# Performance work log

Hardware: AMD Instinct MI355X
Metric: run time of the kernel (lower is better)

Reference implementation:

```python
import jax, jax.numpy as jnp
import numpy as np

# MLP widths: 2 -> 1024 -> 512 -> 256 -> 3, ReLU between layers (not after last)
DIMS = [2, 1024, 512, 256, 3]


def setup_inputs() -> dict:
    key = jax.random.key(0)
    ks = jax.random.split(key, 1 + 2 * (len(DIMS) - 1))
    N = 262144  # 512x512 pixel coordinates
    inp = {"coord": jax.random.normal(ks[0], (N, 2), dtype=jnp.float32)}
    # PyTorch nn.Linear default init: U(-1/sqrt(fan_in), 1/sqrt(fan_in))
    for i, (fi, fo) in enumerate(zip(DIMS[:-1], DIMS[1:])):
        bound = 1.0 / np.sqrt(fi)
        inp[f"W{i}"] = jax.random.uniform(ks[1 + 2 * i], (fi, fo), jnp.float32, -bound, bound)
        inp[f"b{i}"] = jax.random.uniform(ks[2 + 2 * i], (fo,), jnp.float32, -bound, bound)
    return inp


def reference(coord, W0, b0, W1, b1, W2, b2, W3, b3):
    h = jax.nn.relu(coord @ W0 + b0)   # [N, 1024]
    h = jax.nn.relu(h @ W1 + b1)       # [N, 512]
    h = jax.nn.relu(h @ W2 + b2)       # [N, 256]
    return h @ W3 + b3                 # [N, 3]
```

## Files before the change

kernel.cpp:

```cpp
#include <hip/hip_runtime.h>


typedef _Float16 f16;
typedef f16 f16x8 __attribute__((ext_vector_type(8)));
typedef f16 f16x4 __attribute__((ext_vector_type(4)));
typedef float f32x16 __attribute__((ext_vector_type(16)));

#define MFMA(a, b, c) __builtin_amdgcn_mfma_f32_32x32x16_f16((a), (b), (c), 0, 0, 0)

#define U_W1F 0
#define U_W2F 65536
#define U_W3F 81920
#define U_P0F 82944
#define U_B1F 84992
#define U_B2F 86016
#define U_TOTAL 86528

__global__ void prep_kernel(const float* __restrict__ W0, const float* __restrict__ b0,
                            const float* __restrict__ W1, const float* __restrict__ b1,
                            const float* __restrict__ W2, const float* __restrict__ b2,
                            const float* __restrict__ W3, f16* __restrict__ ws)
{
    int u = blockIdx.x * 256 + threadIdx.x;
    if (u >= U_TOTAL) return;
    int lane = u & 63;
    int l31 = lane & 31;
    int q = lane >> 5;
    f16x8 v;
#pragma unroll
    for (int e = 0; e < 8; ++e) v[e] = (f16)0.f;

    if (u < U_W2F) {
        int jt = u >> 12, ks = (u >> 6) & 63;
        int j = jt * 32 + l31;
        int kb = ks * 16 + q * 8;
        const float* p = W1 + (size_t)kb * 512 + j;
#pragma unroll
        for (int e = 0; e < 8; ++e) v[e] = (f16)p[(size_t)e * 512];
    } else if (u < U_W3F) {
        int t = u - U_W2F;
        int jt = t >> 11, ks = (t >> 6) & 31;
        int j = jt * 32 + l31;
        int kb = ks * 16 + q * 8;
        const float* p = W2 + (size_t)kb * 256 + j;
#pragma unroll
        for (int e = 0; e < 8; ++e) v[e] = (f16)p[(size_t)e * 256];
    } else if (u < U_P0F) {
        int t = u - U_W3F;
        int ks = t >> 6;
        int j = l31;
        int kb = ks * 16 + q * 8;
        if (j < 3) {
            const float* p = W3 + (size_t)kb * 3 + j;
#pragma unroll
            for (int e = 0; e < 8; ++e) v[e] = (f16)p[(size_t)e * 3];
        }
    } else if (u < U_B1F) {
        int t = u - U_P0F;
        int jt = t >> 6;
        int j = jt * 32 + l31;
        if (q == 0) {
            float w00 = W0[j], w01 = W0[1024 + j], bb = b0[j];
            f16 w00h = (f16)w00, w01h = (f16)w01, bh = (f16)bb;
            v[0] = w00h; v[1] = w01h; v[2] = bh;
            v[3] = w00h; v[4] = w01h;
            v[5] = (f16)(w00 - (float)w00h);
            v[6] = (f16)(w01 - (float)w01h);
            v[7] = (f16)(bb - (float)bh);
        }
    } else if (u < U_B2F) {
        int t = u - U_B1F;
        int jt = t >> 6;
        int j = jt * 32 + l31;
        if (q == 0) v[0] = (f16)b1[j];
    } else {
        int t = u - U_B2F;
        int jt = t >> 6;
        int j = jt * 32 + l31;
        if (q == 0) v[0] = (f16)b2[j];
    }
    ((f16x8*)ws)[u] = v;
}

__device__ __forceinline__ void slab_write4(unsigned char* lds, int m, int dw ,
                                            int rs, f16x4 val)
{
    int s = (m & 15) << 1;
    *(f16x4*)(lds + (size_t)m * rs + (size_t)((dw ^ s) << 2)) = val;
}

__device__ __forceinline__ f16x8 slab_read8(const unsigned char* lds, int m, int dw ,
                                            int rs)
{
    int s = (m & 15) << 1;
    f16x4 lo = *(const f16x4*)(lds + (size_t)m * rs + (size_t)((dw ^ s) << 2));
    f16x4 hi = *(const f16x4*)(lds + (size_t)m * rs + (size_t)(((dw + 2) ^ s) << 2));
    union { f16x8 v; f16x4 p[2]; } u;
    u.p[0] = lo; u.p[1] = hi;
    return u.v;
}

__device__ __forceinline__ f16x4 relu_pack4(const f32x16& d, int t)
{
    f16x4 pk;
#pragma unroll
    for (int r = 0; r < 4; ++r) {
        float v = d[4 * t + r];
        pk[r] = (f16)(v > 0.f ? v : 0.f);
    }
    return pk;
}

__global__ __launch_bounds__(512)
void mlp_kernel(const float* __restrict__ X, const float* __restrict__ b3,
                const f16* __restrict__ ws, float* __restrict__ out)
{
    const f16x8* W1F = (const f16x8*)ws + U_W1F;
    const f16x8* W2F = (const f16x8*)ws + U_W2F;
    const f16x8* W3F = (const f16x8*)ws + U_W3F;
    const f16x8* P0F = (const f16x8*)ws + U_P0F;
    const f16x8* B1F = (const f16x8*)ws + U_B1F;
    const f16x8* B2F = (const f16x8*)ws + U_B2F;

    __shared__ __align__(16) unsigned char lds[65536];

    const int tid  = threadIdx.x;
    const int w    = tid >> 6;
    const int lane = tid & 63;
    const int l31  = lane & 31;
    const int q    = lane >> 5;
    const size_t rowbase = (size_t)blockIdx.x * 64;

    f32x16 zero16;
#pragma unroll
    for (int i = 0; i < 16; ++i) zero16[i] = 0.f;

    f16x8 ones;
#pragma unroll
    for (int e = 0; e < 8; ++e) ones[e] = (f16)0.f;
    if (q == 0) ones[0] = (f16)1.f;

    f16x8 xfrag[2];
#pragma unroll
    for (int mt = 0; mt < 2; ++mt) {
        f16x8 v;
#pragma unroll
        for (int e = 0; e < 8; ++e) v[e] = (f16)0.f;
        if (q == 0) {
            float2 xv = ((const float2*)X)[rowbase + mt * 32 + l31];
            f16 x0h = (f16)xv.x, x1h = (f16)xv.y;
            v[0] = x0h; v[1] = x1h; v[2] = (f16)1.f;
            v[3] = (f16)(xv.x - (float)x0h);
            v[4] = (f16)(xv.y - (float)x1h);
            v[5] = x0h; v[6] = x1h; v[7] = (f16)1.f;
        }
        xfrag[mt] = v;
    }

    const int jt0 = w * 2;
    f32x16 acc2[2][2];
#pragma unroll
    for (int ji = 0; ji < 2; ++ji) {
        f32x16 binit = MFMA(B1F[(jt0 + ji) * 64 + lane], ones, zero16);
        acc2[ji][0] = binit;
        acc2[ji][1] = binit;
    }

    for (int c = 0; c < 4; ++c) {
        {
            f16x8 af1 = P0F[(c * 8 + w) * 64 + lane];
            int kb = w * 32 + 4 * q;
#pragma unroll
            for (int mt = 0; mt < 2; ++mt) {
                f32x16 d = MFMA(af1, xfrag[mt], zero16);
                int m = mt * 32 + l31;
#pragma unroll
                for (int t = 0; t < 4; ++t)
                    slab_write4(lds, m, (kb + 8 * t) >> 1, 512, relu_pack4(d, t));
            }
        }
        __syncthreads();
#pragma unroll 4
        for (int ks = 0; ks < 16; ++ks) {
            int ksg = c * 16 + ks;
            f16x8 af0 = W1F[(jt0 * 64 + ksg) * 64 + lane];
            f16x8 af1 = W1F[((jt0 + 1) * 64 + ksg) * 64 + lane];
            int dw = (ks * 16 + q * 8) >> 1;
            f16x8 bf0 = slab_read8(lds, l31, dw, 512);
            f16x8 bf1 = slab_read8(lds, 32 + l31, dw, 512);
            acc2[0][0] = MFMA(af0, bf0, acc2[0][0]);
            acc2[0][1] = MFMA(af0, bf1, acc2[0][1]);
            acc2[1][0] = MFMA(af1, bf0, acc2[1][0]);
            acc2[1][1] = MFMA(af1, bf1, acc2[1][1]);
        }
        __syncthreads();
    }

#pragma unroll
    for (int ji = 0; ji < 2; ++ji) {
        int jb = (jt0 + ji) * 32 + 4 * q;
#pragma unroll
        for (int mt = 0; mt < 2; ++mt) {
            int m = mt * 32 + l31;
#pragma unroll
            for (int t = 0; t < 4; ++t)
                slab_write4(lds, m, (jb + 8 * t) >> 1, 1024,
                            relu_pack4(acc2[ji][mt], t));
        }
    }
    __syncthreads();

    f32x16 acc3[2];
    {
        f32x16 binit = MFMA(B2F[w * 64 + lane], ones, zero16);
        acc3[0] = binit;
        acc3[1] = binit;
    }
#pragma unroll 4
    for (int ks = 0; ks < 32; ++ks) {
        f16x8 af = W2F[(w * 32 + ks) * 64 + lane];
        int dw = (ks * 16 + q * 8) >> 1;
        f16x8 bf0 = slab_read8(lds, l31, dw, 1024);
        f16x8 bf1 = slab_read8(lds, 32 + l31, dw, 1024);
        acc3[0] = MFMA(af, bf0, acc3[0]);
        acc3[1] = MFMA(af, bf1, acc3[1]);
    }
    __syncthreads();

    {
        int jb = w * 32 + 4 * q;
#pragma unroll
        for (int mt = 0; mt < 2; ++mt) {
            int m = mt * 32 + l31;
#pragma unroll
            for (int t = 0; t < 4; ++t)
                slab_write4(lds, m, (jb + 8 * t) >> 1, 512,
                            relu_pack4(acc3[mt], t));
        }
    }
    __syncthreads();

    if (w < 2) {
        f32x16 acc4 = zero16;
#pragma unroll 4
        for (int ks = 0; ks < 16; ++ks) {
            f16x8 af = W3F[ks * 64 + lane];
            f16x8 bf = slab_read8(lds, w * 32 + l31, (ks * 16 + q * 8) >> 1, 512);
            acc4 = MFMA(af, bf, acc4);
        }
        if (q == 0) {
            size_t gm = rowbase + w * 32 + l31;
            out[gm * 3 + 0] = acc4[0] + b3[0];
            out[gm * 3 + 1] = acc4[1] + b3[1];
            out[gm * 3 + 2] = acc4[2] + b3[2];
        }
    }
}

extern "C" void kernel_launch(void* const* d_in, const int* in_sizes, int n_in,
                              void* d_out, int out_size, void* d_ws, size_t ws_size,
                              hipStream_t stream)
{
    const float* X  = (const float*)d_in[0];
    const float* W0 = (const float*)d_in[1];
    const float* b0 = (const float*)d_in[2];
    const float* W1 = (const float*)d_in[3];
    const float* b1 = (const float*)d_in[4];
    const float* W2 = (const float*)d_in[5];
    const float* b2 = (const float*)d_in[6];
    const float* W3 = (const float*)d_in[7];
    const float* b3 = (const float*)d_in[8];
    f16* ws = (f16*)d_ws;

    int N = in_sizes[0] / 2;
    int nblk = N / 64;

    prep_kernel<<<(U_TOTAL + 255) / 256, 256, 0, stream>>>(W0, b0, W1, b1, W2, b2, W3, ws);
    mlp_kernel<<<nblk, 512, 0, stream>>>(X, b3, ws, (float*)d_out);
}
```

Baseline: 422.6 us.

## Process 128 rows per block to double W1 fragment reuse in layer two

Each block now handles 128 rows instead of 64. Layer-1/2 accumulators cover four M-tiles, so every W1 fragment loaded from global memory feeds twice as many MFMAs. Layers three and four then run in two 64-row halves that reuse the existing LDS slab. This halves the global weight traffic per row for the largest GEMM, at the cost of more accumulator registers, a 128-row LDS slab, and extra barriers. Launch bounds now request two blocks per CU, which may force spilling.

```diff
diff --git a/kernel.cpp b/kernel.cpp
--- a/kernel.cpp
+++ b/kernel.cpp
@@ -111,7 +111,7 @@
     return pk;
 }
 
-__global__ __launch_bounds__(512)
+__global__ __launch_bounds__(512, 2)
 void mlp_kernel(const float* __restrict__ X, const float* __restrict__ b3,
                 const f16* __restrict__ ws, float* __restrict__ out)
 {
@@ -129,7 +129,7 @@
     const int lane = tid & 63;
     const int l31  = lane & 31;
     const int q    = lane >> 5;
-    const size_t rowbase = (size_t)blockIdx.x * 64;
+    const size_t rowbase = (size_t)blockIdx.x * 128;
 
     f32x16 zero16;
 #pragma unroll
@@ -140,9 +140,9 @@
     for (int e = 0; e < 8; ++e) ones[e] = (f16)0.f;
     if (q == 0) ones[0] = (f16)1.f;
 
-    f16x8 xfrag[2];
-#pragma unroll
-    for (int mt = 0; mt < 2; ++mt) {
+    f16x8 xfrag[4];
+#pragma unroll
+    for (int mt = 0; mt < 4; ++mt) {
         f16x8 v;
 #pragma unroll
         for (int e = 0; e < 8; ++e) v[e] = (f16)0.f;
@@ -158,12 +158,12 @@
     }
 
     const int jt0 = w * 2;
-    f32x16 acc2[2][2];
+    f32x16 acc2[2][4];
 #pragma unroll
     for (int ji = 0; ji < 2; ++ji) {
         f32x16 binit = MFMA(B1F[(jt0 + ji) * 64 + lane], ones, zero16);
-        acc2[ji][0] = binit;
-        acc2[ji][1] = binit;
+#pragma unroll
+        for (int mt = 0; mt < 4; ++mt) acc2[ji][mt] = binit;
     }
 
     for (int c = 0; c < 4; ++c) {
@@ -171,7 +171,7 @@
             f16x8 af1 = P0F[(c * 8 + w) * 64 + lane];
             int kb = w * 32 + 4 * q;
 #pragma unroll
-            for (int mt = 0; mt < 2; ++mt) {
+            for (int mt = 0; mt < 4; ++mt) {
                 f32x16 d = MFMA(af1, xfrag[mt], zero16);
                 int m = mt * 32 + l31;
 #pragma unroll
@@ -188,72 +188,79 @@
             int dw = (ks * 16 + q * 8) >> 1;
             f16x8 bf0 = slab_read8(lds, l31, dw, 512);
             f16x8 bf1 = slab_read8(lds, 32 + l31, dw, 512);
+            f16x8 bf2 = slab_read8(lds, 64 + l31, dw, 512);
+            f16x8 bf3 = slab_read8(lds, 96 + l31, dw, 512);
             acc2[0][0] = MFMA(af0, bf0, acc2[0][0]);
             acc2[0][1] = MFMA(af0, bf1, acc2[0][1]);
+            acc2[0][2] = MFMA(af0, bf2, acc2[0][2]);
+            acc2[0][3] = MFMA(af0, bf3, acc2[0][3]);
             acc2[1][0] = MFMA(af1, bf0, acc2[1][0]);
             acc2[1][1] = MFMA(af1, bf1, acc2[1][1]);
-        }
-        __syncthreads();
-    }
-
-#pragma unroll
-    for (int ji = 0; ji < 2; ++ji) {
-        int jb = (jt0 + ji) * 32 + 4 * q;
-#pragma unroll
-        for (int mt = 0; mt < 2; ++mt) {
-            int m = mt * 32 + l31;
-#pragma unroll
-            for (int t = 0; t < 4; ++t)
-                slab_write4(lds, m, (jb + 8 * t) >> 1, 1024,
-                            relu_pack4(acc2[ji][mt], t));
-        }
-    }
-    __syncthreads();
-
-    f32x16 acc3[2];
-    {
-        f32x16 binit = MFMA(B2F[w * 64 + lane], ones, zero16);
-        acc3[0] = binit;
-        acc3[1] = binit;
-    }
+            acc2[1][2] = MFMA(af1, bf2, acc2[1][2]);
+            acc2[1][3] = MFMA(af1, bf3, acc2[1][3]);
+        }
+        __syncthreads();
+    }
+
+#pragma unroll
+    for (int mh = 0; mh < 2; ++mh) {
+#pragma unroll
+        for (int ji = 0; ji < 2; ++ji) {
+            int jb = (jt0 + ji) * 32 + 4 * q;
+#pragma unroll
+            for (int u = 0; u < 2; ++u) {
+                int m = u * 32 + l31;
+#pragma unroll
+                for (int t = 0; t < 4; ++t)
+                    slab_write4(lds, m, (jb + 8 * t) >> 1, 1024,
+                                relu_pack4(acc2[ji][mh * 2 + u], t));
+            }
+        }
+        __syncthreads();
+        f32x16 acc3[2];
+        {
+            f32x16 binit = MFMA(B2F[w * 64 + lane], ones, zero16);
+            acc3[0] = binit;
+            acc3[1] = binit;
+        }
 #pragma unroll 4
-    for (int ks = 0; ks < 32; ++ks) {
-        f16x8 af = W2F[(w * 32 + ks) * 64 + lane];
-        int dw = (ks * 16 + q * 8) >> 1;
-        f16x8 bf0 = slab_read8(lds, l31, dw, 1024);
-        f16x8 bf1 = slab_read8(lds, 32 + l31, dw, 1024);
-        acc3[0] = MFMA(af, bf0, acc3[0]);
-        acc3[1] = MFMA(af, bf1, acc3[1]);
-    }
-    __syncthreads();
-
-    {
-        int jb = w * 32 + 4 * q;
-#pragma unroll
-        for (int mt = 0; mt < 2; ++mt) {
-            int m = mt * 32 + l31;
-#pragma unroll
-            for (int t = 0; t < 4; ++t)
-                slab_write4(lds, m, (jb + 8 * t) >> 1, 512,
-                            relu_pack4(acc3[mt], t));
-        }
-    }
-    __syncthreads();
-
-    if (w < 2) {
-        f32x16 acc4 = zero16;
+        for (int ks = 0; ks < 32; ++ks) {
+            f16x8 af = W2F[(w * 32 + ks) * 64 + lane];
+            int dw = (ks * 16 + q * 8) >> 1;
+            f16x8 bf0 = slab_read8(lds, l31, dw, 1024);
+            f16x8 bf1 = slab_read8(lds, 32 + l31, dw, 1024);
+            acc3[0] = MFMA(af, bf0, acc3[0]);
+            acc3[1] = MFMA(af, bf1, acc3[1]);
+        }
+        __syncthreads();
+        {
+            int jb = w * 32 + 4 * q;
+#pragma unroll
+            for (int u = 0; u < 2; ++u) {
+                int m = u * 32 + l31;
+#pragma unroll
+                for (int t = 0; t < 4; ++t)
+                    slab_write4(lds, m, (jb + 8 * t) >> 1, 512,
+                                relu_pack4(acc3[u], t));
+            }
+        }
+        __syncthreads();
+        if (w < 2) {
+            f32x16 acc4 = zero16;
 #pragma unroll 4
-        for (int ks = 0; ks < 16; ++ks) {
-            f16x8 af = W3F[ks * 64 + lane];
-            f16x8 bf = slab_read8(lds, w * 32 + l31, (ks * 16 + q * 8) >> 1, 512);
-            acc4 = MFMA(af, bf, acc4);
-        }
-        if (q == 0) {
-            size_t gm = rowbase + w * 32 + l31;
-            out[gm * 3 + 0] = acc4[0] + b3[0];
-            out[gm * 3 + 1] = acc4[1] + b3[1];
-            out[gm * 3 + 2] = acc4[2] + b3[2];
-        }
+            for (int ks = 0; ks < 16; ++ks) {
+                f16x8 af = W3F[ks * 64 + lane];
+                f16x8 bf = slab_read8(lds, w * 32 + l31, (ks * 16 + q * 8) >> 1, 512);
+                acc4 = MFMA(af, bf, acc4);
+            }
+            if (q == 0) {
+                size_t gm = rowbase + mh * 64 + w * 32 + l31;
+                out[gm * 3 + 0] = acc4[0] + b3[0];
+                out[gm * 3 + 1] = acc4[1] + b3[1];
+                out[gm * 3 + 2] = acc4[2] + b3[2];
+            }
+        }
+        __syncthreads();
     }
 }
 
@@ -273,7 +280,7 @@
     f16* ws = (f16*)d_ws;
 
     int N = in_sizes[0] / 2;
-    int nblk = N / 64;
+    int nblk = N / 128;
 
     prep_kernel<<<(U_TOTAL + 255) / 256, 256, 0, stream>>>(W0, b0, W1, b1, W2, b2, W3, ws);
     mlp_kernel<<<nblk, 512, 0, stream>>>(X, b3, ws, (float*)d_out);
```

Result: faster. 408.6 us (-3.3%).

## Double rows per block with 1024-thread blocks and padded LDS rows

Applied to the files above, without the earlier changes.

Each block now processes 128 rows with 16 waves, two row-halves sharing the same weight-fragment tiles per wave index, and uses dynamic shared memory sized for padded row strides. The XOR swizzle on LDS addresses is replaced by row padding (520/1028/516 bytes) with precomputed base pointers, which removes address arithmetic. Unroll factors drop from 4 to 2. The larger block (about 131KB of LDS) lowers the number of resident blocks per CU and makes barriers span more waves, while weight reads from L2 are not shared across waves.

```diff
diff --git a/kernel.cpp b/kernel.cpp
--- a/kernel.cpp
+++ b/kernel.cpp
@@ -7,6 +7,11 @@
 typedef float f32x16 __attribute__((ext_vector_type(16)));
 
 #define MFMA(a, b, c) __builtin_amdgcn_mfma_f32_32x32x16_f16((a), (b), (c), 0, 0, 0)
+
+#define RS1 520
+#define RS2 1028
+#define RS3 516
+#define SLABSZ (128 * RS2)
 
 #define U_W1F 0
 #define U_W2F 65536
@@ -82,24 +87,6 @@
     ((f16x8*)ws)[u] = v;
 }
 
-__device__ __forceinline__ void slab_write4(unsigned char* lds, int m, int dw ,
-                                            int rs, f16x4 val)
-{
-    int s = (m & 15) << 1;
-    *(f16x4*)(lds + (size_t)m * rs + (size_t)((dw ^ s) << 2)) = val;
-}
-
-__device__ __forceinline__ f16x8 slab_read8(const unsigned char* lds, int m, int dw ,
-                                            int rs)
-{
-    int s = (m & 15) << 1;
-    f16x4 lo = *(const f16x4*)(lds + (size_t)m * rs + (size_t)((dw ^ s) << 2));
-    f16x4 hi = *(const f16x4*)(lds + (size_t)m * rs + (size_t)(((dw + 2) ^ s) << 2));
-    union { f16x8 v; f16x4 p[2]; } u;
-    u.p[0] = lo; u.p[1] = hi;
-    return u.v;
-}
-
 __device__ __forceinline__ f16x4 relu_pack4(const f32x16& d, int t)
 {
     f16x4 pk;
@@ -111,7 +98,15 @@
     return pk;
 }
 
-__global__ __launch_bounds__(512)
+__device__ __forceinline__ f16x8 aff_read8(const unsigned char* p, int byteoff)
+{
+    union { f16x8 v; f16x4 h[2]; } u;
+    u.h[0] = *(const f16x4*)(p + byteoff);
+    u.h[1] = *(const f16x4*)(p + byteoff + 8);
+    return u.v;
+}
+
+__global__ __launch_bounds__(1024)
 void mlp_kernel(const float* __restrict__ X, const float* __restrict__ b3,
                 const f16* __restrict__ ws, float* __restrict__ out)
 {
@@ -122,18 +117,16 @@
     const f16x8* B1F = (const f16x8*)ws + U_B1F;
     const f16x8* B2F = (const f16x8*)ws + U_B2F;
 
-    __shared__ __align__(16) unsigned char lds[65536];
+    extern __shared__ __align__(16) unsigned char lds[];
 
     const int tid  = threadIdx.x;
     const int w    = tid >> 6;
     const int lane = tid & 63;
     const int l31  = lane & 31;
     const int q    = lane >> 5;
-    const size_t rowbase = (size_t)blockIdx.x * 64;
-
-    f32x16 zero16;
-#pragma unroll
-    for (int i = 0; i < 16; ++i) zero16[i] = 0.f;
+    const int wl   = w & 7;
+    const int mth  = w >> 3;
+    const size_t rowbase = (size_t)blockIdx.x * 128;
 
     f16x8 ones;
 #pragma unroll
@@ -142,52 +135,55 @@
 
     f16x8 xfrag[2];
 #pragma unroll
-    for (int mt = 0; mt < 2; ++mt) {
+    for (int u = 0; u < 2; ++u) {
         f16x8 v;
 #pragma unroll
         for (int e = 0; e < 8; ++e) v[e] = (f16)0.f;
         if (q == 0) {
-            float2 xv = ((const float2*)X)[rowbase + mt * 32 + l31];
+            float2 xv = ((const float2*)X)[rowbase + (mth * 2 + u) * 32 + l31];
             f16 x0h = (f16)xv.x, x1h = (f16)xv.y;
             v[0] = x0h; v[1] = x1h; v[2] = (f16)1.f;
             v[3] = (f16)(xv.x - (float)x0h);
             v[4] = (f16)(xv.y - (float)x1h);
             v[5] = x0h; v[6] = x1h; v[7] = (f16)1.f;
         }
-        xfrag[mt] = v;
-    }
-
-    const int jt0 = w * 2;
+        xfrag[u] = v;
+    }
+
+    const int jt0 = wl * 2;
     f32x16 acc2[2][2];
 #pragma unroll
     for (int ji = 0; ji < 2; ++ji) {
-        f32x16 binit = MFMA(B1F[(jt0 + ji) * 64 + lane], ones, zero16);
+        f32x16 z = {};
+        f32x16 binit = MFMA(B1F[(jt0 + ji) * 64 + lane], ones, z);
         acc2[ji][0] = binit;
         acc2[ji][1] = binit;
     }
 
+    const unsigned char* pb = lds + (mth * 64 + l31) * RS1 + q * 16;
+    unsigned char* pw = lds + (size_t)(mth * 64 + l31) * RS1 + wl * 64 + q * 8;
+
     for (int c = 0; c < 4; ++c) {
         {
-            f16x8 af1 = P0F[(c * 8 + w) * 64 + lane];
-            int kb = w * 32 + 4 * q;
-#pragma unroll
-            for (int mt = 0; mt < 2; ++mt) {
-                f32x16 d = MFMA(af1, xfrag[mt], zero16);
-                int m = mt * 32 + l31;
+            f16x8 afp = P0F[(c * 8 + wl) * 64 + lane];
+#pragma unroll
+            for (int u = 0; u < 2; ++u) {
+                f32x16 z = {};
+                f32x16 d = MFMA(afp, xfrag[u], z);
 #pragma unroll
                 for (int t = 0; t < 4; ++t)
-                    slab_write4(lds, m, (kb + 8 * t) >> 1, 512, relu_pack4(d, t));
+                    *(f16x4*)(pw + u * (32 * RS1) + t * 16) = relu_pack4(d, t);
             }
         }
         __syncthreads();
-#pragma unroll 4
+        const f16x8* pa0 = W1F + ((size_t)jt0 * 64 + c * 16) * 64 + lane;
+        const f16x8* pa1 = pa0 + 64 * 64;
+#pragma unroll 2
         for (int ks = 0; ks < 16; ++ks) {
-            int ksg = c * 16 + ks;
-            f16x8 af0 = W1F[(jt0 * 64 + ksg) * 64 + lane];
-            f16x8 af1 = W1F[((jt0 + 1) * 64 + ksg) * 64 + lane];
-            int dw = (ks * 16 + q * 8) >> 1;
-            f16x8 bf0 = slab_read8(lds, l31, dw, 512);
-            f16x8 bf1 = slab_read8(lds, 32 + l31, dw, 512);
+            f16x8 af0 = pa0[ks * 64];
+            f16x8 af1 = pa1[ks * 64];
+            f16x8 bf0 = aff_read8(pb, ks * 32);
+            f16x8 bf1 = aff_read8(pb, 32 * RS1 + ks * 32);
             acc2[0][0] = MFMA(af0, bf0, acc2[0][0]);
             acc2[0][1] = MFMA(af0, bf1, acc2[0][1]);
             acc2[1][0] = MFMA(af1, bf0, acc2[1][0]);
@@ -196,56 +192,60 @@
         __syncthreads();
     }
 
-#pragma unroll
-    for (int ji = 0; ji < 2; ++ji) {
-        int jb = (jt0 + ji) * 32 + 4 * q;
-#pragma unroll
-        for (int mt = 0; mt < 2; ++mt) {
-            int m = mt * 32 + l31;
-#pragma unroll
-            for (int t = 0; t < 4; ++t)
-                slab_write4(lds, m, (jb + 8 * t) >> 1, 1024,
-                            relu_pack4(acc2[ji][mt], t));
+    {
+#pragma unroll
+        for (int ji = 0; ji < 2; ++ji) {
+            unsigned char* ph = lds + (size_t)(jt0 + ji) * 64 + q * 8;
+#pragma unroll
+            for (int mt = 0; mt < 2; ++mt) {
+                unsigned char* phm = ph + (size_t)(mth * 64 + mt * 32 + l31) * RS2;
+#pragma unroll
+                for (int t = 0; t < 4; ++t)
+                    *(f16x4*)(phm + t * 16) = relu_pack4(acc2[ji][mt], t);
+            }
         }
     }
     __syncthreads();
 
     f32x16 acc3[2];
     {
-        f32x16 binit = MFMA(B2F[w * 64 + lane], ones, zero16);
+        f32x16 z = {};
+        f32x16 binit = MFMA(B2F[wl * 64 + lane], ones, z);
         acc3[0] = binit;
         acc3[1] = binit;
     }
-#pragma unroll 4
-    for (int ks = 0; ks < 32; ++ks) {
-        f16x8 af = W2F[(w * 32 + ks) * 64 + lane];
-        int dw = (ks * 16 + q * 8) >> 1;
-        f16x8 bf0 = slab_read8(lds, l31, dw, 1024);
-        f16x8 bf1 = slab_read8(lds, 32 + l31, dw, 1024);
-        acc3[0] = MFMA(af, bf0, acc3[0]);
-        acc3[1] = MFMA(af, bf1, acc3[1]);
+    {
+        const unsigned char* pb3 = lds + (size_t)(mth * 64 + l31) * RS2 + q * 16;
+#pragma unroll 2
+        for (int ks = 0; ks < 32; ++ks) {
+            f16x8 af = W2F[(wl * 32 + ks) * 64 + lane];
+            f16x8 bf0 = aff_read8(pb3, ks * 32);
+            f16x8 bf1 = aff_read8(pb3, 32 * RS2 + ks * 32);
+            acc3[0] = MFMA(af, bf0, acc3[0]);
+            acc3[1] = MFMA(af, bf1, acc3[1]);
+        }
     }
     __syncthreads();
 
     {
-        int jb = w * 32 + 4 * q;
+        unsigned char* ph = lds + (size_t)wl * 64 + q * 8;
 #pragma unroll
         for (int mt = 0; mt < 2; ++mt) {
-            int m = mt * 32 + l31;
+            unsigned char* phm = ph + (size_t)(mth * 64 + mt * 32 + l31) * RS3;
 #pragma unroll
             for (int t = 0; t < 4; ++t)
-                slab_write4(lds, m, (jb + 8 * t) >> 1, 512,
-                            relu_pack4(acc3[mt], t));
+                *(f16x4*)(phm + t * 16) = relu_pack4(acc3[mt], t);
         }
     }
     __syncthreads();
 
-    if (w < 2) {
-        f32x16 acc4 = zero16;
-#pragma unroll 4
+    if (w < 4) {
+        const unsigned char* pb4 = lds + (size_t)(w * 32 + l31) * RS3 + q * 16;
+        f32x16 acc4 = {};
+#pragma unroll 2
         for (int ks = 0; ks < 16; ++ks) {
             f16x8 af = W3F[ks * 64 + lane];
-            f16x8 bf = slab_read8(lds, w * 32 + l31, (ks * 16 + q * 8) >> 1, 512);
+            f16x8 bf = aff_read8(pb4, ks * 32);
             acc4 = MFMA(af, bf, acc4);
         }
         if (q == 0) {
@@ -273,8 +273,11 @@
     f16* ws = (f16*)d_ws;
 
     int N = in_sizes[0] / 2;
-    int nblk = N / 64;
+    int nblk = N / 128;
+
+    (void)hipFuncSetAttribute((const void*)mlp_kernel,
+                              hipFuncAttributeMaxDynamicSharedMemorySize, SLABSZ);
 
     prep_kernel<<<(U_TOTAL + 255) / 256, 256, 0, stream>>>(W0, b0, W1, b1, W2, b2, W3, ws);
-    mlp_kernel<<<nblk, 512, 0, stream>>>(X, b3, ws, (float*)d_out);
-}
+    mlp_kernel<<<nblk, 1024, SLABSZ, stream>>>(X, b3, ws, (float*)d_out);
+}
```

After: 882.2 us. +108.7%, slower.
